# Kernel tuning notes

Hardware: AMD Instinct MI355X
Metric: run time of the kernel (lower is better)

## Reference

```python
import jax, jax.numpy as jnp
import numpy as np

N = 50000      # nodes
E = 800000     # edges (avg degree 16)
IN = 128       # in_size
OUT = 64       # out_size
H = 32         # hidden_size
WIDTH = 3      # width
SCALE = 0.05


def _laplacian(x, src, tgt, n):
    # normalized Laplacian action: out[t] = sum_{edges into t} (x[t] - x[s]) / deg(t)
    deg = jax.ops.segment_sum(jnp.ones((tgt.shape[0],), x.dtype), tgt, num_segments=n)
    fac = 1.0 / deg[tgt]                       # [E], deg>=1 for any target that appears
    msg = (x[tgt] - x[src]) * fac[:, None]     # [E, F]
    return jax.ops.segment_sum(msg, tgt, num_segments=n)


def _grouped_linear(x, Wg, bg):
    # Conv1d(kernel=1, groups=width) == per-group linear
    n = x.shape[0]
    xg = x.reshape(n, WIDTH, -1)               # [N, width, h_in]
    out = jnp.einsum('nwh,who->nwo', xg, Wg) + bg
    return out.reshape(n, -1)                  # [N, width*h_out]


def setup_inputs() -> dict:
    key = jax.random.key(0)
    ks = jax.random.split(key, 14)
    data = jax.random.normal(ks[0], (N, IN), jnp.float32)
    src = jax.random.randint(ks[1], (E,), 0, N)
    tgt = jnp.sort(jax.random.randint(ks[2], (E,), 0, N))
    # preprocess ConvSkip: Linear(in, hidden*width) + Linear(in, hidden*width)
    W_pre = jax.random.normal(ks[3], (IN, H * WIDTH), jnp.float32) * SCALE
    b_pre = jnp.zeros((H * WIDTH,), jnp.float32)
    T_pre = jax.random.normal(ks[4], (IN, H * WIDTH), jnp.float32) * SCALE
    bT_pre = jnp.zeros((H * WIDTH,), jnp.float32)
    # middle WideConvSkip (depth-2 = 1 block): grouped conv [width, H, H]
    W_blk = jax.random.normal(ks[5], (WIDTH, H, H), jnp.float32) * SCALE
    b_blk = jnp.zeros((WIDTH, H), jnp.float32)
    T_blk = jax.random.normal(ks[6], (IN, H * WIDTH), jnp.float32) * SCALE
    bT_blk = jnp.zeros((H * WIDTH,), jnp.float32)
    # postprocess WideConvSkip: grouped conv [width, H, OUT]
    W_post = jax.random.normal(ks[7], (WIDTH, H, OUT), jnp.float32) * SCALE
    b_post = jnp.zeros((WIDTH, OUT), jnp.float32)
    T_post = jax.random.normal(ks[8], (IN, OUT * WIDTH), jnp.float32) * SCALE
    bT_post = jnp.zeros((OUT * WIDTH,), jnp.float32)
    return {"data": data, "src": src, "tgt": tgt,
            "W_pre": W_pre, "b_pre": b_pre, "T_pre": T_pre, "bT_pre": bT_pre,
            "W_blk": W_blk, "b_blk": b_blk, "T_blk": T_blk, "bT_blk": bT_blk,
            "W_post": W_post, "b_post": b_post, "T_post": T_post, "bT_post": bT_post}


def reference(data, src, tgt, W_pre, b_pre, T_pre, bT_pre,
              W_blk, b_blk, T_blk, bT_blk,
              W_post, b_post, T_post, bT_post):
    n = data.shape[0]
    # preprocess ConvSkip: sigma(L f(x) + g(x))
    out = data @ W_pre + b_pre
    out = _laplacian(out, src, tgt, n)
    out = jax.nn.relu(out + data @ T_pre + bT_pre)       # [N, H*width]
    # middle WideConvSkip (depth - 2 = 1)
    h = _grouped_linear(out, W_blk, b_blk)
    h = _laplacian(h, src, tgt, n)
    out = jax.nn.relu(h + data @ T_blk + bT_blk)          # [N, H*width]
    # postprocess WideConvSkip
    h = _grouped_linear(out, W_post, b_post)
    h = _laplacian(h, src, tgt, n)
    out = jax.nn.relu(h + data @ T_post + bT_post)        # [N, OUT*width]
    # reshape(N, -1, width) then adaptive_avg_pool1d(., 1) == mean over width
    out = out.reshape(n, -1, WIDTH)
    return out.mean(axis=-1, keepdims=True)               # [N, OUT, 1]
```

## Files before the change

### kernel.cpp

```cpp
#include <hip/hip_runtime.h>
#include <cstdint>
#include <cstddef>

#define N_NODES 50000
#define E_EDGES 800000
#define IN_F    128
#define PCOLS   512

typedef unsigned short ushortT;
typedef unsigned int   uintT;
typedef __attribute__((ext_vector_type(8))) short s8v;
typedef __attribute__((ext_vector_type(4))) float f4v;
typedef __attribute__((ext_vector_type(2))) float f2v;

__device__ __forceinline__ float bflo(uintT u){ union{uintT i;float f;}c; c.i=u<<16; return c.f; }
__device__ __forceinline__ float bfhi(uintT u){ union{uintT i;float f;}c; c.i=u&0xFFFF0000u; return c.f; }
__device__ __forceinline__ ushortT f2bfu(float f){
    union{float f;uintT u;}c; c.f=f;
    uintT r = c.u + 0x7FFF + ((c.u>>16)&1);
    return (ushortT)(r>>16);
}
__device__ __forceinline__ uintT pack2(float a, float b){
    return (uintT)f2bfu(a) | ((uintT)f2bfu(b) << 16);
}

__global__ void prep1(const float* __restrict__ A,
                      const float* __restrict__ Wp,  const float* __restrict__ bp,
                      const float* __restrict__ Tp,  const float* __restrict__ bTp,
                      const float* __restrict__ Tb,  const float* __restrict__ bTb,
                      const float* __restrict__ Tpo, const float* __restrict__ bTpo,
                      const float* __restrict__ Wpost,
                      const int* __restrict__ tgt,
                      ushortT* __restrict__ Wb, float* __restrict__ bcat,
                      float2* __restrict__ Wp2,
                      ushortT* __restrict__ Ab, int* __restrict__ row_ptr,
                      ushortT* __restrict__ Pb, ushortT* __restrict__ rb1,
                      ushortT* __restrict__ rb2)
{
    int gid = blockIdx.x * 256 + threadIdx.x;
    {
        size_t off = (size_t)gid * 8;
        float4 v0 = *(const float4*)(A + off);
        float4 v1 = *(const float4*)(A + off + 4);
        uint4 u;
        u.x = pack2(v0.x, v0.y); u.y = pack2(v0.z, v0.w);
        u.z = pack2(v1.x, v1.y); u.w = pack2(v1.z, v1.w);
        *(uint4*)(Ab + off) = u;
    }
    if (gid < IN_F * PCOLS) {
        int k = gid >> 9;
        int c = gid & 511;
        float v;
        if      (c < 96)  v = Wp [k*96  + c];
        else if (c < 192) v = Tp [k*96  + (c-96)];
        else if (c < 288) v = Tb [k*96  + (c-192)];
        else if (c < 480) v = Tpo[k*192 + (c-288)];
        else              v = 0.f;
        Wb[(size_t)c*IN_F + k] = f2bfu(v);
        if (k == 0) {
            float b;
            if      (c < 96)  b = bp  [c];
            else if (c < 192) b = bTp [c-96];
            else if (c < 288) b = bTb [c-192];
            else if (c < 480) b = bTpo[c-288];
            else              b = 0.f;
            bcat[c] = b;
        }
        if (gid < 3*16*64) {
            int w = gid >> 10, r = gid & 1023;
            int i2 = r >> 6, j = r & 63;
            Wp2[gid] = make_float2(Wpost[(w*32 + 2*i2)*64 + j],
                                   Wpost[(w*32 + 2*i2 + 1)*64 + j]);
        }
    }
    if (gid < 96) {
        Pb [(size_t)N_NODES*PCOLS + gid] = 0;
        rb1[(size_t)N_NODES*96   + gid] = 0;
        rb2[(size_t)N_NODES*96   + gid] = 0;
    }
    if (gid <= N_NODES) {
        int lo = 0, hi = E_EDGES;
        while (lo < hi) {
            int mid = (lo + hi) >> 1;
            if (tgt[mid] < gid) lo = mid + 1; else hi = mid;
        }
        row_ptr[gid] = lo;
    }
}

__global__ __launch_bounds__(256, 2) void gemm_mfma(const ushortT* __restrict__ Ab,
                                                    const ushortT* __restrict__ Wb,
                                                    const float* __restrict__ bcat,
                                                    ushortT* __restrict__ Pb, int M)
{
    __shared__ ushortT Asl[128][72];
    __shared__ ushortT Bsl[128][72];
    int tid = threadIdx.x;
    int nb = blockIdx.x * 128;
    int mb = blockIdx.y * 128;
    int wv = tid >> 6, lane = tid & 63;
    int wm = wv >> 1, wn = wv & 1;
    int cl = lane & 15, q = lane >> 4;

    f4v acc[4][4];
    #pragma unroll
    for (int i = 0; i < 4; ++i)
        #pragma unroll
        for (int j = 0; j < 4; ++j) acc[i][j] = (f4v)0.f;

    for (int kt = 0; kt < IN_F; kt += 64) {
        if (kt) __syncthreads();
        #pragma unroll
        for (int r = 0; r < 4; ++r) {
            int idx = tid + 256*r;
            int row = idx >> 3, qq = idx & 7;
            int gm = mb + row;
            uint4 v = make_uint4(0,0,0,0);
            if (gm < M) v = *(const uint4*)(Ab + (size_t)gm*IN_F + kt + qq*8);
            *(uint4*)(&Asl[row][qq*8]) = v;
        }
        #pragma unroll
        for (int r = 0; r < 4; ++r) {
            int idx = tid + 256*r;
            int row = idx >> 3, qq = idx & 7;
            uint4 v = *(const uint4*)(Wb + (size_t)(nb+row)*IN_F + kt + qq*8);
            *(uint4*)(&Bsl[row][qq*8]) = v;
        }
        __syncthreads();
        #pragma unroll
        for (int ks = 0; ks < 2; ++ks) {
            int ko = ks*32 + q*8;
            s8v af[4], bf[4];
            #pragma unroll
            for (int mt = 0; mt < 4; ++mt)
                af[mt] = *(const s8v*)(&Asl[wm*64 + mt*16 + cl][ko]);
            #pragma unroll
            for (int nt = 0; nt < 4; ++nt)
                bf[nt] = *(const s8v*)(&Bsl[wn*64 + nt*16 + cl][ko]);
            #pragma unroll
            for (int mt = 0; mt < 4; ++mt)
                #pragma unroll
                for (int nt = 0; nt < 4; ++nt)
                    acc[mt][nt] = __builtin_amdgcn_mfma_f32_16x16x32_bf16(af[mt], bf[nt], acc[mt][nt], 0, 0, 0);
        }
    }

    #pragma unroll
    for (int nt = 0; nt < 4; ++nt) {
        int gn = nb + wn*64 + nt*16 + cl;
        float bv = bcat[gn];
        #pragma unroll
        for (int mt = 0; mt < 4; ++mt) {
            int gm0 = mb + wm*64 + mt*16 + q*4;
            #pragma unroll
            for (int r = 0; r < 4; ++r) {
                int gm = gm0 + r;
                if (gm < M) Pb[(size_t)gm*PCOLS + gn] = f2bfu(acc[mt][nt][r] + bv);
            }
        }
    }
}

#define GATHER96(Xb, lo, deg, sv, pL, STRB, sx, sy)                               \
    float sx, sy;                                                                 \
    {                                                                             \
        f2v c0={0.f,0.f}, c1={0.f,0.f}, c2={0.f,0.f}, c3={0.f,0.f};               \
        int dmax = deg < 64 ? deg : 64;                                           \
        _Pragma("unroll 1")                                                       \
        for (int w_ = 0; w_ < dmax; w_ += 16) {                                   \
            uintT u[16];                                                          \
            _Pragma("unroll")                                                     \
            for (int kk = 0; kk < 16; ++kk) {                                     \
                int off = __builtin_amdgcn_readlane(sv, w_ + kk);                 \
                const char* rp = (const char*)(Xb) + off;                         \
                u[kk] = *(const uintT*)(rp + 4*pL);                               \
            }                                                                     \
            _Pragma("unroll")                                                     \
            for (int kk = 0; kk < 16; ++kk) {                                     \
                f2v v_; v_.x = bflo(u[kk]); v_.y = bfhi(u[kk]);                   \
                switch (kk & 3) {                                                 \
                    case 0: c0 += v_; break;                                      \
                    case 1: c1 += v_; break;                                      \
                    case 2: c2 += v_; break;                                      \
                    default:c3 += v_; break;                                      \
                }                                                                 \
            }                                                                     \
        }                                                                         \
        if (deg > 64) {                                                           \
            _Pragma("unroll 1")                                                   \
            for (int j_ = lo + 64; j_ < lo + deg; ++j_) {                         \
                int off = src[j_] * (STRB);                                       \
                const char* rp = (const char*)(Xb) + off;                         \
                uintT u0 = *(const uintT*)(rp + 4*pL);                            \
                f2v v_; v_.x = bflo(u0); v_.y = bfhi(u0);                         \
                c0 += v_;                                                         \
            }                                                                     \
        }                                                                         \
        f2v cs_ = (c0 + c1) + (c2 + c3);                                          \
        sx = cs_.x; sy = cs_.y;                                                   \
    }

#define MAKE_SV(lo, deg, lane, STRB, sv)                                          \
    int sv;                                                                       \
    {                                                                             \
        int e_ = (lo) + (lane);                                                   \
        if (e_ > E_EDGES - 1) e_ = E_EDGES - 1;                                   \
        int sn_ = src[e_];                                                        \
        sv = ((lane) < (deg) ? sn_ : N_NODES) * (STRB);                           \
    }

__global__ __launch_bounds__(256) void lap1(
    const ushortT* __restrict__ Pb,
    const int* __restrict__ src, const int* __restrict__ row_ptr,
    ushortT* __restrict__ rb1)
{
    int lane = threadIdx.x & 63;
    int t  = __builtin_amdgcn_readfirstlane((blockIdx.x << 2) + (threadIdx.x >> 6));
    int lo = __builtin_amdgcn_readfirstlane(row_ptr[t]);
    int deg = __builtin_amdgcn_readfirstlane(row_ptr[t+1]) - lo;
    int pL = lane < 48 ? lane : 0;
    MAKE_SV(lo, deg, lane, 2*PCOLS, sv)
    uintT ux = *(const uintT*)(Pb + (size_t)t*PCOLS + 2*pL);
    uintT zu = *(const uintT*)(Pb + (size_t)t*PCOLS + 96 + 2*pL);

    GATHER96(Pb, lo, deg, sv, pL, 2*PCOLS, sx, sy)

    float inv = deg > 0 ? 1.f/(float)deg : 0.f;
    float mf  = deg > 0 ? 1.f : 0.f;
    if (lane < 48) {
        float ox = fmaxf(mf*bflo(ux) - sx*inv + bflo(zu), 0.f);
        float oy = fmaxf(mf*bfhi(ux) - sy*inv + bfhi(zu), 0.f);
        *(uintT*)(rb1 + (size_t)t*96 + 2*pL) = pack2(ox, oy);
    }
}

__global__ __launch_bounds__(256) void lap2(
    const ushortT* __restrict__ Xb,
    const ushortT* __restrict__ Pb,
    const int* __restrict__ src, const int* __restrict__ row_ptr,
    const float* __restrict__ Wblk,
    ushortT* __restrict__ rb2)
{
    __shared__ float wS[3*32*32];
    for (int i = threadIdx.x; i < 3072; i += 256) wS[i] = Wblk[i];
    __syncthreads();

    int lane = threadIdx.x & 63;
    int wvw  = threadIdx.x >> 6;
    int pL = lane < 48 ? lane : 0;
    int w  = pL >> 4;
    int jj = pL & 15;
    const float2* wc = ((const float2*)wS) + (w*512 + jj);

    #pragma unroll 1
    for (int it = 0; it < 4; ++it) {
        int t  = __builtin_amdgcn_readfirstlane(blockIdx.x*16 + it*4 + wvw);
        int lo = __builtin_amdgcn_readfirstlane(row_ptr[t]);
        int deg = __builtin_amdgcn_readfirstlane(row_ptr[t+1]) - lo;
        MAKE_SV(lo, deg, lane, 192, sv)
        uintT ux = *(const uintT*)(Xb + (size_t)t*96 + 2*pL);
        uintT zu = *(const uintT*)(Pb + (size_t)t*PCOLS + 192 + 2*pL);

        GATHER96(Xb, lo, deg, sv, pL, 192, sx, sy)

        float inv = deg > 0 ? 1.f/(float)deg : 0.f;
        float mf  = deg > 0 ? 1.f : 0.f;
        float Lx = mf*bflo(ux) - sx*inv;
        float Ly = mf*bfhi(ux) - sy*inv;

        float accx = 0.f, accy = 0.f;
        #pragma unroll
        for (int d = 0; d < 16; ++d) {
            int sl = w*16 + d;
            float ax = __shfl(Lx, sl);
            float ay = __shfl(Ly, sl);
            float2 wa = wc[(2*d)*16];
            float2 wb = wc[(2*d+1)*16];
            accx = fmaf(ax, wa.x, accx); accx = fmaf(ay, wb.x, accx);
            accy = fmaf(ax, wa.y, accy); accy = fmaf(ay, wb.y, accy);
        }
        if (lane < 48) {
            float ox = fmaxf(accx + bflo(zu), 0.f);
            float oy = fmaxf(accy + bfhi(zu), 0.f);
            *(uintT*)(rb2 + (size_t)t*96 + 2*pL) = pack2(ox, oy);
        }
    }
}

__global__ __launch_bounds__(256) void lap3(
    const ushortT* __restrict__ Xb,
    const ushortT* __restrict__ Pb,
    const int* __restrict__ src, const int* __restrict__ row_ptr,
    const float2* __restrict__ Wp2,
    float* __restrict__ out)
{
    __shared__ float2 wS[3*16*64];
    __shared__ float  sm[4][96];
    for (int i = threadIdx.x; i < 3072; i += 256) wS[i] = Wp2[i];
    __syncthreads();

    int lane = threadIdx.x & 63;
    int wvw  = threadIdx.x >> 6;
    int pL = lane < 48 ? lane : 0;
    const float2* wl = wS + lane;

    #pragma unroll 1
    for (int it = 0; it < 4; ++it) {
        int t  = __builtin_amdgcn_readfirstlane(blockIdx.x*16 + it*4 + wvw);
        int lo = __builtin_amdgcn_readfirstlane(row_ptr[t]);
        int deg = __builtin_amdgcn_readfirstlane(row_ptr[t+1]) - lo;
        MAKE_SV(lo, deg, lane, 192, sv)
        uintT ux = *(const uintT*)(Xb + (size_t)t*96 + 2*pL);
        float z0 = bflo((uintT)Pb[(size_t)t*PCOLS + 288 + lane]);
        float z1 = bflo((uintT)Pb[(size_t)t*PCOLS + 352 + lane]);
        float z2 = bflo((uintT)Pb[(size_t)t*PCOLS + 416 + lane]);

        GATHER96(Xb, lo, deg, sv, pL, 192, sx, sy)

        float inv = deg > 0 ? 1.f/(float)deg : 0.f;
        float mf  = deg > 0 ? 1.f : 0.f;
        float Lx = mf*bflo(ux) - sx*inv;
        float Ly = mf*bfhi(ux) - sy*inv;

        if (lane < 48) {
            sm[wvw][2*pL]     = Lx;
            sm[wvw][2*pL + 1] = Ly;
        }
        __builtin_amdgcn_wave_barrier();

        float a0 = 0.f, a1 = 0.f, a2 = 0.f;
        #pragma unroll
        for (int w2 = 0; w2 < 3; ++w2) {
            float acc = 0.f;
            #pragma unroll
            for (int i2 = 0; i2 < 16; ++i2) {
                float2 iv = *(const float2*)(&sm[wvw][w2*32 + 2*i2]);
                float2 p  = wl[(w2*16 + i2)*64];
                acc = fmaf(iv.x, p.x, acc);
                acc = fmaf(iv.y, p.y, acc);
            }
            if (w2 == 0) a0 = acc; else if (w2 == 1) a1 = acc; else a2 = acc;
        }
        __builtin_amdgcn_wave_barrier();

        float o0 = fmaxf(a0 + z0, 0.f);
        float o1 = fmaxf(a1 + z1, 0.f);
        float o2 = fmaxf(a2 + z2, 0.f);
        float r = 0.f;
        #pragma unroll
        for (int q = 0; q < 3; ++q) {
            int c = 3*lane + q;
            int sl = c & 63, wsel = c >> 6;
            float v0 = __shfl(o0, sl);
            float v1 = __shfl(o1, sl);
            float v2 = __shfl(o2, sl);
            r += (wsel == 0) ? v0 : ((wsel == 1) ? v1 : v2);
        }
        out[(size_t)t*64 + lane] = r * (1.0f/3.0f);
    }
}

extern "C" void kernel_launch(void* const* d_in, const int* in_sizes, int n_in,
                              void* d_out, int out_size, void* d_ws, size_t ws_size,
                              hipStream_t stream)
{
    const float* data    = (const float*)d_in[0];
    const int*   src     = (const int*)  d_in[1];
    const int*   tgt     = (const int*)  d_in[2];
    const float* W_pre   = (const float*)d_in[3];
    const float* b_pre   = (const float*)d_in[4];
    const float* T_pre   = (const float*)d_in[5];
    const float* bT_pre  = (const float*)d_in[6];
    const float* W_blk   = (const float*)d_in[7];
    const float* b_blk   = (const float*)d_in[8];
    const float* T_blk   = (const float*)d_in[9];
    const float* bT_blk  = (const float*)d_in[10];
    const float* W_post  = (const float*)d_in[11];
    const float* b_post  = (const float*)d_in[12];
    const float* T_post  = (const float*)d_in[13];
    const float* bT_post = (const float*)d_in[14];
    float* out = (float*)d_out;

    float*   ws      = (float*)d_ws;
    float*   bcat    = ws;
    float2*  Wp2     = (float2*)(bcat + 512);
    int*     row_ptr = (int*)(Wp2 + 3*16*64);
    ushortT* Pb      = (ushortT*)(row_ptr + 50008);
    ushortT* rb1     = Pb  + (size_t)(N_NODES+1) * PCOLS;
    ushortT* rb2     = rb1 + (size_t)(N_NODES+1) * 96;
    ushortT* Ab      = rb2 + (size_t)(N_NODES+1) * 96;
    ushortT* Wb      = Ab  + (size_t)N_NODES * IN_F;

    prep1<<<(N_NODES*IN_F/8)/256, 256, 0, stream>>>(
        data, W_pre, b_pre, T_pre, bT_pre, T_blk, bT_blk, T_post, bT_post,
        W_post, tgt, Wb, bcat, Wp2, Ab, row_ptr, Pb, rb1, rb2);

    dim3 gg(PCOLS/128, (N_NODES + 127)/128);
    gemm_mfma<<<gg, 256, 0, stream>>>(Ab, Wb, bcat, Pb, N_NODES);

    lap1<<<N_NODES/4, 256, 0, stream>>>(Pb, src, row_ptr, rb1);
    lap2<<<N_NODES/16, 256, 0, stream>>>(rb1, Pb, src, row_ptr, W_blk, rb2);
    lap3<<<N_NODES/16, 256, 0, stream>>>(rb2, Pb, src, row_ptr, Wp2, out);
}
```

Baseline: 285.8 us.

## Restructure bf16 GEMM: full-K B tile in LDS, direct A loads, XCD-aware block mapping

The GEMM kernel now keeps the whole 128x128 B tile (full K) in LDS and loads A fragments straight from global memory into registers, which removes the K-loop, its barriers and the A staging. Blocks are launched as a 1D grid remapped so that each XCD gets a contiguous range of M rows, which should improve L2 locality. The output goes through LDS so it can be written as coalesced 16-byte stores, and launch bounds are raised to allow more resident blocks. Direct A loads are less coalesced, and 1568 blocks covers 392 M tiles for only 391 needed, which the M bound check handles. This kernel is a small part of a pipeline that the gather-bound Laplacian kernels dominate.

Measured after the change: 267.3 us. -6.5%, faster.

```diff
diff --git a/kernel.cpp b/kernel.cpp
--- a/kernel.cpp
+++ b/kernel.cpp
@@ -88,75 +88,82 @@
     }
 }
 
-__global__ __launch_bounds__(256, 2) void gemm_mfma(const ushortT* __restrict__ Ab,
+__global__ __launch_bounds__(256, 4) void gemm_mfma(const ushortT* __restrict__ Ab,
                                                     const ushortT* __restrict__ Wb,
                                                     const float* __restrict__ bcat,
                                                     ushortT* __restrict__ Pb, int M)
 {
-    __shared__ ushortT Asl[128][72];
-    __shared__ ushortT Bsl[128][72];
+    __shared__ ushortT Bsl[128][136];
     int tid = threadIdx.x;
-    int nb = blockIdx.x * 128;
-    int mb = blockIdx.y * 128;
+    int i = blockIdx.x;
+    int xcd = i & 7, j = i >> 3;
+    int nb = (j & 3) * 128;
+    int mb = (xcd * 49 + (j >> 2)) * 128;
     int wv = tid >> 6, lane = tid & 63;
     int wm = wv >> 1, wn = wv & 1;
     int cl = lane & 15, q = lane >> 4;
 
+    #pragma unroll
+    for (int r = 0; r < 8; ++r) {
+        int idx = tid + 256*r;
+        int row = idx >> 4, qq = idx & 15;
+        uint4 v = *(const uint4*)(Wb + (size_t)(nb+row)*IN_F + qq*8);
+        *(uint4*)(&Bsl[row][qq*8]) = v;
+    }
+    __syncthreads();
+
     f4v acc[4][4];
     #pragma unroll
-    for (int i = 0; i < 4; ++i)
-        #pragma unroll
-        for (int j = 0; j < 4; ++j) acc[i][j] = (f4v)0.f;
-
-    for (int kt = 0; kt < IN_F; kt += 64) {
-        if (kt) __syncthreads();
-        #pragma unroll
-        for (int r = 0; r < 4; ++r) {
-            int idx = tid + 256*r;
-            int row = idx >> 3, qq = idx & 7;
-            int gm = mb + row;
-            uint4 v = make_uint4(0,0,0,0);
-            if (gm < M) v = *(const uint4*)(Ab + (size_t)gm*IN_F + kt + qq*8);
-            *(uint4*)(&Asl[row][qq*8]) = v;
-        }
-        #pragma unroll
-        for (int r = 0; r < 4; ++r) {
-            int idx = tid + 256*r;
-            int row = idx >> 3, qq = idx & 7;
-            uint4 v = *(const uint4*)(Wb + (size_t)(nb+row)*IN_F + kt + qq*8);
-            *(uint4*)(&Bsl[row][qq*8]) = v;
-        }
-        __syncthreads();
-        #pragma unroll
-        for (int ks = 0; ks < 2; ++ks) {
-            int ko = ks*32 + q*8;
-            s8v af[4], bf[4];
-            #pragma unroll
-            for (int mt = 0; mt < 4; ++mt)
-                af[mt] = *(const s8v*)(&Asl[wm*64 + mt*16 + cl][ko]);
+    for (int a = 0; a < 4; ++a)
+        #pragma unroll
+        for (int b = 0; b < 4; ++b) acc[a][b] = (f4v)0.f;
+
+    int gmBase = mb + wm*64;
+    #pragma unroll
+    for (int ks = 0; ks < 4; ++ks) {
+        int ko = ks*32 + q*8;
+        s8v af[4], bf[4];
+        #pragma unroll
+        for (int mt = 0; mt < 4; ++mt) {
+            int gm = gmBase + mt*16 + cl;
+            uint4 va = make_uint4(0,0,0,0);
+            if (gm < M) va = *(const uint4*)(Ab + (size_t)gm*IN_F + ko);
+            af[mt] = *(s8v*)&va;
+        }
+        #pragma unroll
+        for (int nt = 0; nt < 4; ++nt)
+            bf[nt] = *(const s8v*)(&Bsl[wn*64 + nt*16 + cl][ko]);
+        #pragma unroll
+        for (int mt = 0; mt < 4; ++mt)
             #pragma unroll
             for (int nt = 0; nt < 4; ++nt)
-                bf[nt] = *(const s8v*)(&Bsl[wn*64 + nt*16 + cl][ko]);
-            #pragma unroll
-            for (int mt = 0; mt < 4; ++mt)
-                #pragma unroll
-                for (int nt = 0; nt < 4; ++nt)
-                    acc[mt][nt] = __builtin_amdgcn_mfma_f32_16x16x32_bf16(af[mt], bf[nt], acc[mt][nt], 0, 0, 0);
-        }
-    }
+                acc[mt][nt] = __builtin_amdgcn_mfma_f32_16x16x32_bf16(af[mt], bf[nt], acc[mt][nt], 0, 0, 0);
+    }
+
+    __syncthreads();
 
     #pragma unroll
     for (int nt = 0; nt < 4; ++nt) {
-        int gn = nb + wn*64 + nt*16 + cl;
-        float bv = bcat[gn];
+        int cn = wn*64 + nt*16 + cl;
+        float bv = bcat[nb + cn];
         #pragma unroll
         for (int mt = 0; mt < 4; ++mt) {
-            int gm0 = mb + wm*64 + mt*16 + q*4;
+            int rm0 = wm*64 + mt*16 + q*4;
             #pragma unroll
-            for (int r = 0; r < 4; ++r) {
-                int gm = gm0 + r;
-                if (gm < M) Pb[(size_t)gm*PCOLS + gn] = f2bfu(acc[mt][nt][r] + bv);
-            }
+            for (int r = 0; r < 4; ++r)
+                Bsl[rm0 + r][cn] = f2bfu(acc[mt][nt][r] + bv);
+        }
+    }
+    __syncthreads();
+
+    #pragma unroll
+    for (int p = 0; p < 8; ++p) {
+        int idx = tid + 256*p;
+        int row = idx >> 4, sg = idx & 15;
+        int gm = mb + row;
+        if (gm < M) {
+            uint4 v = *(const uint4*)(&Bsl[row][sg*8]);
+            *(uint4*)(Pb + (size_t)gm*PCOLS + nb + sg*8) = v;
         }
     }
 }
@@ -395,8 +402,7 @@
         data, W_pre, b_pre, T_pre, bT_pre, T_blk, bT_blk, T_post, bT_post,
         W_post, tgt, Wb, bcat, Wp2, Ab, row_ptr, Pb, rb1, rb2);
 
-    dim3 gg(PCOLS/128, (N_NODES + 127)/128);
-    gemm_mfma<<<gg, 256, 0, stream>>>(Ab, Wb, bcat, Pb, N_NODES);
+    gemm_mfma<<<1568, 256, 0, stream>>>(Ab, Wb, bcat, Pb, N_NODES);
 
     lap1<<<N_NODES/4, 256, 0, stream>>>(Pb, src, row_ptr, rb1);
     lap2<<<N_NODES/16, 256, 0, stream>>>(rb1, Pb, src, row_ptr, W_blk, rb2);
```
